# Kernel tuning notes

Measured on AMD Instinct MI355X. Metric: run time of the kernel, lower is better.

## Reference

```python
import jax, jax.numpy as jnp
import numpy as np

B, S, E, H, O = 256, 2048, 64, 128, 1


def setup_inputs() -> dict:
    key = jax.random.key(0)
    ks = jax.random.split(key, 12)
    s_e = 1.0 / np.sqrt(E)
    s_h = 1.0 / np.sqrt(H)
    return {
        "inputs": jax.random.normal(ks[0], (B, S, E), dtype=jnp.float32),
        "time_interval": jax.random.uniform(ks[1], (B, S), dtype=jnp.float32),
        "W_all": jax.random.uniform(ks[2], (4 * H, H), jnp.float32, -s_h, s_h),
        "b_all": jax.random.uniform(ks[3], (4 * H,), jnp.float32, -s_h, s_h),
        "U_all": jax.random.uniform(ks[4], (4 * H, E), jnp.float32, -s_e, s_e),
        "b_u": jax.random.uniform(ks[5], (4 * H,), jnp.float32, -s_e, s_e),
        "W_d": jax.random.uniform(ks[6], (H, H), jnp.float32, -s_h, s_h),
        "b_d": jax.random.uniform(ks[7], (H,), jnp.float32, -s_h, s_h),
        "W_out": jax.random.uniform(ks[8], (O, H), jnp.float32, -s_h, s_h),
        "b_out": jax.random.uniform(ks[9], (O,), jnp.float32, -s_h, s_h),
    }


def reference(inputs, time_interval, W_all, b_all, U_all, b_u, W_d, b_d, W_out, b_out):
    b, seq, _ = inputs.shape
    hdim = W_d.shape[0]
    # Precompute input projection for all timesteps: [S, B, 4H]
    x_proj = jnp.einsum('bse,fe->sbf', inputs, U_all) + b_u
    dt = time_interval.T  # [S, B]

    def step(carry, xs):
        h, c = carry
        xp, d = xs  # xp: [B,4H], d: [B]
        c_s1 = jnp.tanh(c @ W_d.T + b_d)
        c_adj = (c - c_s1) + c_s1 * d[:, None]
        outs = h @ W_all.T + b_all + xp
        f, i, o, c_tmp = jnp.split(outs, 4, axis=1)
        f = jax.nn.sigmoid(f)
        i = jax.nn.sigmoid(i)
        o = jax.nn.sigmoid(o)
        c_tmp = jax.nn.sigmoid(c_tmp)
        c_new = f * c_adj + i * c_tmp
        h_new = o * jnp.tanh(c_new)
        return (h_new, c_new), h_new

    h0 = jnp.zeros((b, hdim), dtype=inputs.dtype)
    c0 = jnp.zeros((b, hdim), dtype=inputs.dtype)
    _, hs = jax.lax.scan(step, (h0, c0), (x_proj, dt))  # hs: [S, B, H]
    # out(h_s) summed over s, then flatten to [B*O]
    outs = jnp.einsum('sbh,oh->sbo', hs, W_out) + b_out  # [S,B,O]
    return outs.sum(axis=0).reshape(-1)
```

## Files before the change

kernel.cpp:

```cpp
#include <hip/hip_runtime.h>
#include <math.h>

#define BB 256
#define SS 2048
#define EE 64
#define HH 128

typedef _Float16 half2_t __attribute__((ext_vector_type(2)));
typedef unsigned int uint2v __attribute__((ext_vector_type(2)));

#if defined(__has_builtin)
#if __has_builtin(__builtin_amdgcn_fdot2)
#define HAVE_FDOT2 1
#endif
#if __has_builtin(__builtin_amdgcn_update_dpp)
#define HAVE_DPP 1
#endif
#if __has_builtin(__builtin_amdgcn_permlane32_swap)
#define HAVE_PL32 1
#endif
#if __has_builtin(__builtin_amdgcn_exp2f)
#define EXP2F(x) __builtin_amdgcn_exp2f(x)
#else
#define EXP2F(x) exp2f(x)
#endif
#if __has_builtin(__builtin_amdgcn_rcpf)
#define RCPF(x) __builtin_amdgcn_rcpf(x)
#else
#define RCPF(x) (1.0f / (x))
#endif
#else
#define EXP2F(x) exp2f(x)
#define RCPF(x) (1.0f / (x))
#endif

__device__ __forceinline__ float dot2f(half2_t a, half2_t b, float c) {
#ifdef HAVE_FDOT2
    return __builtin_amdgcn_fdot2(a, b, c, false);
#else
    return c + (float)a.x * (float)b.x + (float)a.y * (float)b.y;
#endif
}

__device__ __forceinline__ float dpp_xor1(float v) {
#ifdef HAVE_DPP
    int r = __builtin_amdgcn_update_dpp(0, __float_as_int(v), 0xB1, 0xF, 0xF, true);
    return __int_as_float(r);
#else
    return __shfl_xor(v, 1, 64);
#endif
}
__device__ __forceinline__ float dpp_xor2(float v) {
#ifdef HAVE_DPP
    int r = __builtin_amdgcn_update_dpp(0, __float_as_int(v), 0x4E, 0xF, 0xF, true);
    return __int_as_float(r);
#else
    return __shfl_xor(v, 2, 64);
#endif
}

__device__ __forceinline__ float xhalf_recv(float a, float b, bool lower) {
#ifdef HAVE_PL32
    uint2v r = __builtin_amdgcn_permlane32_swap(__float_as_int(a), __float_as_int(b), false, false);
    return __int_as_float((int)(lower ? r.y : r.x));
#else
    float ra = __shfl_xor(a, 32, 64);
    float rb = __shfl_xor(b, 32, 64);
    return lower ? ra : rb;
#endif
}

__device__ __forceinline__ float sigm_f(float x) {
    float e = EXP2F(-1.442695041f * x);
    return RCPF(1.0f + e);
}
__device__ __forceinline__ float tanh_f(float x) {
    float e = EXP2F(2.885390082f * x);
    return 1.0f - 2.0f * RCPF(1.0f + e);
}

__global__ __attribute__((amdgpu_flat_work_group_size(512, 512)))
__attribute__((amdgpu_waves_per_eu(2, 2)))
void tlstm_fused8_kernel(
    const float* __restrict__ inputs,
    const float* __restrict__ time_interval,
    const float* __restrict__ W_all,
    const float* __restrict__ b_all,
    const float* __restrict__ U_all,
    const float* __restrict__ b_u,
    const float* __restrict__ W_d,
    const float* __restrict__ b_d,
    const float* __restrict__ W_out,
    const float* __restrict__ b_out,
    float* __restrict__ out)
{
    const int b  = blockIdx.x;
    const int t  = threadIdx.x;
    const int wv = t >> 6;
    const int lh = (t >> 5) & 1;
    const int k  = (t >> 2) & 7;
    const int m  = t & 3;
    const int L  = m + 4 * lh;
    const bool lower = (lh == 0);

    const int un_base = 16 * wv + 2 * k;
    const int my_un   = un_base + lh;

    __shared__ __align__(16) _Float16 sh_h[2][HH];
    __shared__ __align__(16) _Float16 sh_c[2][HH];
    __shared__ __align__(16) _Float16 sh_x[2][EE];
    __shared__ float sh_red[HH];

    half2_t wg[8][8];
    half2_t ug[8][4];
    half2_t wd[2][8];
    float   biasr, bd_r, wout_r;
    {
        #pragma unroll
        for (int uu = 0; uu < 2; ++uu) {
            #pragma unroll
            for (int q = 0; q < 4; ++q) {
                const int j   = q + 4 * uu;
                const int row = (un_base + uu) + 128 * q;
                const float4* pw = (const float4*)(W_all + (size_t)row * HH + 16 * L);
                #pragma unroll
                for (int i = 0; i < 4; ++i) {
                    float4 v = pw[i];
                    half2_t h0, h1;
                    h0.x = (_Float16)v.x; h0.y = (_Float16)v.y;
                    h1.x = (_Float16)v.z; h1.y = (_Float16)v.w;
                    wg[j][2*i]   = h0;
                    wg[j][2*i+1] = h1;
                }
                const float4* pu = (const float4*)(U_all + (size_t)row * EE + 8 * L);
                #pragma unroll
                for (int i = 0; i < 2; ++i) {
                    float4 v = pu[i];
                    half2_t h0, h1;
                    h0.x = (_Float16)v.x; h0.y = (_Float16)v.y;
                    h1.x = (_Float16)v.z; h1.y = (_Float16)v.w;
                    ug[j][2*i]   = h0;
                    ug[j][2*i+1] = h1;
                }
            }
            const int rowd = un_base + uu;
            const float4* pd = (const float4*)(W_d + (size_t)rowd * HH + 16 * L);
            #pragma unroll
            for (int i = 0; i < 4; ++i) {
                float4 v = pd[i];
                half2_t h0, h1;
                h0.x = (_Float16)v.x; h0.y = (_Float16)v.y;
                h1.x = (_Float16)v.z; h1.y = (_Float16)v.w;
                wd[uu][2*i]   = h0;
                wd[uu][2*i+1] = h1;
            }
        }
        const int row_own = my_un + 128 * m;
        biasr  = b_all[row_own] + b_u[row_own];
        bd_r   = b_d[my_un];
        wout_r = W_out[my_un];
    }

    const float* xg   = inputs + (size_t)b * SS * EE;
    const float* drow = time_interval + (size_t)b * SS;

    const int  xl   = t & 63;
    const bool xact = (xl < 8);
    const int  xidx = 8 * wv + (xl & 7);

    const _Float16* hb0 = &sh_h[0][16 * L];
    const _Float16* hb1 = &sh_h[1][16 * L];
    const _Float16* cb0 = &sh_c[0][16 * L];
    const _Float16* cb1 = &sh_c[1][16 * L];
    const _Float16* xr0 = &sh_x[0][8 * L];
    const _Float16* xr1 = &sh_x[1][8 * L];
    _Float16* wxp0 = &sh_x[0][xidx];
    _Float16* wxp1 = &sh_x[1][xidx];
    _Float16* wcp0 = &sh_c[0][my_un];
    _Float16* wcp1 = &sh_c[1][my_un];
    _Float16* whp0 = &sh_h[0][my_un];
    _Float16* whp1 = &sh_h[1][my_un];

    if (t < HH) { sh_h[0][t] = (_Float16)0.f; sh_c[0][t] = (_Float16)0.f; }
    float xcv = 0.f, xld = 0.f;
    if (xact) {
        sh_x[0][xidx] = (_Float16)xg[xidx];
        xcv = xg[EE + xidx];
        xld = xg[2 * EE + xidx];
    }
    float dv0 = drow[0], dv1 = drow[1], dv2 = drow[2];
    float hsum   = 0.f;
    float c_keep = 0.f;
    __syncthreads();

#define TLSTM_STEP(s, CUR, NXT)                                               \
    {                                                                         \
        if (xact) {                                                           \
            *wxp##NXT = (_Float16)xcv;                                        \
            xcv = xld;                                                        \
            const int s3 = ((s) + 3 < SS) ? (s) + 3 : SS - 1;                 \
            xld = xg[(size_t)s3 * EE + xidx];                                 \
        }                                                                     \
        float4 hv0, hv1, cv0, cv1, xv0;                                       \
        {                                                                     \
            const float4* hp = (const float4*)hb##CUR;                        \
            hv0 = hp[0]; hv1 = hp[1];                                         \
            const float4* cp = (const float4*)cb##CUR;                        \
            cv0 = cp[0]; cv1 = cp[1];                                         \
            const float4* xp = (const float4*)xr##CUR;                        \
            xv0 = xp[0];                                                      \
        }                                                                     \
        float a[8] = {0.f,0.f,0.f,0.f,0.f,0.f,0.f,0.f};                       \
        float ad0 = 0.f, ad1 = 0.f;                                           \
        {                                                                     \
            const half2_t* hh = (const half2_t*)&hv0;                         \
            _Pragma("unroll")                                                 \
            for (int p = 0; p < 4; ++p) {                                     \
                _Pragma("unroll")                                             \
                for (int j = 0; j < 8; ++j)                                   \
                    a[j] = dot2f(wg[j][p], hh[p], a[j]);                      \
            }                                                                 \
            hh = (const half2_t*)&hv1;                                        \
            _Pragma("unroll")                                                 \
            for (int p = 0; p < 4; ++p) {                                     \
                _Pragma("unroll")                                             \
                for (int j = 0; j < 8; ++j)                                   \
                    a[j] = dot2f(wg[j][4 + p], hh[p], a[j]);                  \
            }                                                                 \
            const half2_t* xh = (const half2_t*)&xv0;                         \
            _Pragma("unroll")                                                 \
            for (int p = 0; p < 4; ++p) {                                     \
                _Pragma("unroll")                                             \
                for (int j = 0; j < 8; ++j)                                   \
                    a[j] = dot2f(ug[j][p], xh[p], a[j]);                      \
            }                                                                 \
            const half2_t* ch = (const half2_t*)&cv0;                         \
            _Pragma("unroll")                                                 \
            for (int p = 0; p < 4; ++p) {                                     \
                ad0 = dot2f(wd[0][p], ch[p], ad0);                            \
                ad1 = dot2f(wd[1][p], ch[p], ad1);                            \
            }                                                                 \
            ch = (const half2_t*)&cv1;                                        \
            _Pragma("unroll")                                                 \
            for (int p = 0; p < 4; ++p) {                                     \
                ad0 = dot2f(wd[0][4 + p], ch[p], ad0);                        \
                ad1 = dot2f(wd[1][4 + p], ch[p], ad1);                        \
            }                                                                 \
        }                                                                     \
        \
        const bool oddl = (m & 1) != 0;                                       \
        const bool bit2 = (m & 2) != 0;                                       \
        float s0, s1, s2, s3v;                                                \
        {                                                                     \
            float snd, r;                                                     \
            snd = oddl ? a[0] : a[1]; r = dpp_xor1(snd);                      \
            s0 = (oddl ? a[1] : a[0]) + r;                                    \
            snd = oddl ? a[2] : a[3]; r = dpp_xor1(snd);                      \
            s1 = (oddl ? a[3] : a[2]) + r;                                    \
            snd = oddl ? a[4] : a[5]; r = dpp_xor1(snd);                      \
            s2 = (oddl ? a[5] : a[4]) + r;                                    \
            snd = oddl ? a[6] : a[7]; r = dpp_xor1(snd);                      \
            s3v = (oddl ? a[7] : a[6]) + r;                                   \
        }                                                                     \
        float u0v, u1v;                                                       \
        {                                                                     \
            float snd, r;                                                     \
            snd = bit2 ? s0 : s1; r = dpp_xor2(snd);                          \
            u0v = (bit2 ? s1 : s0) + r;                                       \
            snd = bit2 ? s2 : s3v; r = dpp_xor2(snd);                         \
            u1v = (bit2 ? s3v : s2) + r;                                      \
        }                                                                     \
        float g = (lower ? u0v : u1v) + xhalf_recv(u0v, u1v, lower);          \
        \
        float dd = (lower ? ad0 : ad1) + xhalf_recv(ad0, ad1, lower);         \
        dd += dpp_xor2(dd);                                                   \
        dd += dpp_xor1(dd);                                                   \
                  \
        float sg  = sigm_f(g + biasr);                                        \
        float cs1 = tanh_f(bd_r + dd);                                        \
        float sel1 = (m == 2) ? cs1 : sg;                                     \
        float sh2  = dpp_xor2(sel1);                \
        float sh2b = dpp_xor2(sg);                  \
        float dm1  = dv0 - 1.0f;                                              \
        float cadj = __builtin_fmaf(sh2, dm1, c_keep);   \
        float prod = sg * (oddl ? sh2 : cadj);      \
        float cn   = prod + dpp_xor1(prod);            \
        float hn   = sh2b * tanh_f(cn);                \
        c_keep = cn;                                                          \
        hsum  += hn;                                                          \
        if (m == 0) {                                                         \
            *wcp##NXT = (_Float16)cn;                                         \
            *whp##NXT = (_Float16)hn;                                         \
        }                                                                     \
        dv0 = dv1; dv1 = dv2;                                                 \
        const int sd = ((s) + 3 < SS) ? (s) + 3 : SS - 1;                     \
        dv2 = drow[sd];                                                       \
        __syncthreads();                                                      \
    }

    for (int s = 0; s < SS; s += 2) {
        TLSTM_STEP(s,     0, 1)
        TLSTM_STEP(s + 1, 1, 0)
    }
#undef TLSTM_STEP

    if (m == 0) sh_red[my_un] = hsum * wout_r;
    __syncthreads();
    if (t == 0) {
        float acc = 0.f;
        for (int i = 0; i < HH; ++i) acc += sh_red[i];
        out[b] = acc + (float)SS * b_out[0];
    }
}

extern "C" void kernel_launch(void* const* d_in, const int* in_sizes, int n_in,
                              void* d_out, int out_size, void* d_ws, size_t ws_size,
                              hipStream_t stream) {
    const float* inputs        = (const float*)d_in[0];
    const float* time_interval = (const float*)d_in[1];
    const float* W_all         = (const float*)d_in[2];
    const float* b_all         = (const float*)d_in[3];
    const float* U_all         = (const float*)d_in[4];
    const float* b_u           = (const float*)d_in[5];
    const float* W_d           = (const float*)d_in[6];
    const float* b_d           = (const float*)d_in[7];
    const float* W_out         = (const float*)d_in[8];
    const float* b_out         = (const float*)d_in[9];
    float* out = (float*)d_out;

    tlstm_fused8_kernel<<<dim3(BB), dim3(512), 0, stream>>>(
        inputs, time_interval, W_all, b_all, U_all, b_u,
        W_d, b_d, W_out, b_out, out);
}
```

Before: 1.787 ms.

## Split each hidden-unit dot product across 16 lanes with 1024-thread blocks

```diff
diff --git a/kernel.cpp b/kernel.cpp
--- a/kernel.cpp
+++ b/kernel.cpp
@@ -58,6 +58,14 @@
     return __shfl_xor(v, 2, 64);
 #endif
 }
+__device__ __forceinline__ float dpp_ror8(float v) {
+#ifdef HAVE_DPP
+    int r = __builtin_amdgcn_update_dpp(0, __float_as_int(v), 0x128, 0xF, 0xF, true);
+    return __int_as_float(r);
+#else
+    return __shfl_xor(v, 8, 64);
+#endif
+}
 
 __device__ __forceinline__ float xhalf_recv(float a, float b, bool lower) {
 #ifdef HAVE_PL32
@@ -79,9 +87,7 @@
     return 1.0f - 2.0f * RCPF(1.0f + e);
 }
 
-__global__ __attribute__((amdgpu_flat_work_group_size(512, 512)))
-__attribute__((amdgpu_waves_per_eu(2, 2)))
-void tlstm_fused8_kernel(
+__global__ __launch_bounds__(1024, 4) void tlstm_fused16_kernel(
     const float* __restrict__ inputs,
     const float* __restrict__ time_interval,
     const float* __restrict__ W_all,
@@ -96,14 +102,16 @@
 {
     const int b  = blockIdx.x;
     const int t  = threadIdx.x;
+    const int l  = t & 63;
     const int wv = t >> 6;
-    const int lh = (t >> 5) & 1;
-    const int k  = (t >> 2) & 7;
-    const int m  = t & 3;
-    const int L  = m + 4 * lh;
+    const int m  = l & 3;
+    const int q8 = (l >> 3) & 1;
+    const int lh = (l >> 5) & 1;
+    const int gidx = ((l >> 2) & 1) + 2 * ((l >> 4) & 1);
+    const int L  = m + 4 * q8 + 8 * lh;
     const bool lower = (lh == 0);
 
-    const int un_base = 16 * wv + 2 * k;
+    const int un_base = 8 * wv + 2 * gidx;
     const int my_un   = un_base + lh;
 
     __shared__ __align__(16) _Float16 sh_h[2][HH];
@@ -111,9 +119,9 @@
     __shared__ __align__(16) _Float16 sh_x[2][EE];
     __shared__ float sh_red[HH];
 
-    half2_t wg[8][8];
-    half2_t ug[8][4];
-    half2_t wd[2][8];
+    half2_t wg[8][4];
+    half2_t ug[8][2];
+    half2_t wd[2][4];
     float   biasr, bd_r, wout_r;
     {
         #pragma unroll
@@ -122,9 +130,9 @@
             for (int q = 0; q < 4; ++q) {
                 const int j   = q + 4 * uu;
                 const int row = (un_base + uu) + 128 * q;
-                const float4* pw = (const float4*)(W_all + (size_t)row * HH + 16 * L);
+                const float4* pw = (const float4*)(W_all + (size_t)row * HH + 8 * L);
                 #pragma unroll
-                for (int i = 0; i < 4; ++i) {
+                for (int i = 0; i < 2; ++i) {
                     float4 v = pw[i];
                     half2_t h0, h1;
                     h0.x = (_Float16)v.x; h0.y = (_Float16)v.y;
@@ -132,21 +140,20 @@
                     wg[j][2*i]   = h0;
                     wg[j][2*i+1] = h1;
                 }
-                const float4* pu = (const float4*)(U_all + (size_t)row * EE + 8 * L);
-                #pragma unroll
-                for (int i = 0; i < 2; ++i) {
-                    float4 v = pu[i];
+                const float4* pu = (const float4*)(U_all + (size_t)row * EE + 4 * L);
+                {
+                    float4 v = pu[0];
                     half2_t h0, h1;
                     h0.x = (_Float16)v.x; h0.y = (_Float16)v.y;
                     h1.x = (_Float16)v.z; h1.y = (_Float16)v.w;
-                    ug[j][2*i]   = h0;
-                    ug[j][2*i+1] = h1;
+                    ug[j][0] = h0;
+                    ug[j][1] = h1;
                 }
             }
             const int rowd = un_base + uu;
-            const float4* pd = (const float4*)(W_d + (size_t)rowd * HH + 16 * L);
+            const float4* pd = (const float4*)(W_d + (size_t)rowd * HH + 8 * L);
             #pragma unroll
-            for (int i = 0; i < 4; ++i) {
+            for (int i = 0; i < 2; ++i) {
                 float4 v = pd[i];
                 half2_t h0, h1;
                 h0.x = (_Float16)v.x; h0.y = (_Float16)v.y;
@@ -164,16 +171,15 @@
     const float* xg   = inputs + (size_t)b * SS * EE;
     const float* drow = time_interval + (size_t)b * SS;
 
-    const int  xl   = t & 63;
-    const bool xact = (xl < 8);
-    const int  xidx = 8 * wv + (xl & 7);
-
-    const _Float16* hb0 = &sh_h[0][16 * L];
-    const _Float16* hb1 = &sh_h[1][16 * L];
-    const _Float16* cb0 = &sh_c[0][16 * L];
-    const _Float16* cb1 = &sh_c[1][16 * L];
-    const _Float16* xr0 = &sh_x[0][8 * L];
-    const _Float16* xr1 = &sh_x[1][8 * L];
+    const bool xact = (l < 4);
+    const int  xidx = 4 * wv + (l & 3);
+
+    const _Float16* hb0 = &sh_h[0][8 * L];
+    const _Float16* hb1 = &sh_h[1][8 * L];
+    const _Float16* cb0 = &sh_c[0][8 * L];
+    const _Float16* cb1 = &sh_c[1][8 * L];
+    const _Float16* xr0 = &sh_x[0][4 * L];
+    const _Float16* xr1 = &sh_x[1][4 * L];
     _Float16* wxp0 = &sh_x[0][xidx];
     _Float16* wxp1 = &sh_x[1][xidx];
     _Float16* wcp0 = &sh_c[0][my_un];
@@ -201,53 +207,39 @@
             const int s3 = ((s) + 3 < SS) ? (s) + 3 : SS - 1;                 \
             xld = xg[(size_t)s3 * EE + xidx];                                 \
         }                                                                     \
-        float4 hv0, hv1, cv0, cv1, xv0;                                       \
+        float4 hv4, cv4f;                                                     \
+        float2 xv2;                                                           \
         {                                                                     \
-            const float4* hp = (const float4*)hb##CUR;                        \
-            hv0 = hp[0]; hv1 = hp[1];                                         \
-            const float4* cp = (const float4*)cb##CUR;                        \
-            cv0 = cp[0]; cv1 = cp[1];                                         \
-            const float4* xp = (const float4*)xr##CUR;                        \
-            xv0 = xp[0];                                                      \
+            hv4  = *(const float4*)hb##CUR;                                   \
+            cv4f = *(const float4*)cb##CUR;                                   \
+            xv2  = *(const float2*)xr##CUR;                                   \
         }                                                                     \
         float a[8] = {0.f,0.f,0.f,0.f,0.f,0.f,0.f,0.f};                       \
         float ad0 = 0.f, ad1 = 0.f;                                           \
         {                                                                     \
-            const half2_t* hh = (const half2_t*)&hv0;                         \
+            const half2_t* hh = (const half2_t*)&hv4;                         \
             _Pragma("unroll")                                                 \
             for (int p = 0; p < 4; ++p) {                                     \
                 _Pragma("unroll")                                             \
                 for (int j = 0; j < 8; ++j)                                   \
                     a[j] = dot2f(wg[j][p], hh[p], a[j]);                      \
             }                                                                 \
-            hh = (const half2_t*)&hv1;                                        \
+            const half2_t* xh = (const half2_t*)&xv2;                         \
             _Pragma("unroll")                                                 \
-            for (int p = 0; p < 4; ++p) {                                     \
-                _Pragma("unroll")                                             \
-                for (int j = 0; j < 8; ++j)                                   \
-                    a[j] = dot2f(wg[j][4 + p], hh[p], a[j]);                  \
-            }                                                                 \
-            const half2_t* xh = (const half2_t*)&xv0;                         \
-            _Pragma("unroll")                                                 \
-            for (int p = 0; p < 4; ++p) {                                     \
+            for (int p = 0; p < 2; ++p) {                                     \
                 _Pragma("unroll")                                             \
                 for (int j = 0; j < 8; ++j)                                   \
                     a[j] = dot2f(ug[j][p], xh[p], a[j]);                      \
             }                                                                 \
-            const half2_t* ch = (const half2_t*)&cv0;                         \
+            const half2_t* ch = (const half2_t*)&cv4f;                        \
             _Pragma("unroll")                                                 \
             for (int p = 0; p < 4; ++p) {                                     \
                 ad0 = dot2f(wd[0][p], ch[p], ad0);                            \
                 ad1 = dot2f(wd[1][p], ch[p], ad1);                            \
             }                                                                 \
-            ch = (const half2_t*)&cv1;                                        \
-            _Pragma("unroll")                                                 \
-            for (int p = 0; p < 4; ++p) {                                     \
-                ad0 = dot2f(wd[0][4 + p], ch[p], ad0);                        \
-                ad1 = dot2f(wd[1][4 + p], ch[p], ad1);                        \
-            }                                                                 \
-        }                                                                     \
-        \
+        }                                                                     \
+          \
+                   \
         const bool oddl = (m & 1) != 0;                                       \
         const bool bit2 = (m & 2) != 0;                                       \
         float s0, s1, s2, s3v;                                                \
@@ -270,9 +262,12 @@
             snd = bit2 ? s2 : s3v; r = dpp_xor2(snd);                         \
             u1v = (bit2 ? s3v : s2) + r;                                      \
         }                                                                     \
+        u0v += dpp_ror8(u0v);                                                 \
+        u1v += dpp_ror8(u1v);                                                 \
         float g = (lower ? u0v : u1v) + xhalf_recv(u0v, u1v, lower);          \
-        \
+                        \
         float dd = (lower ? ad0 : ad1) + xhalf_recv(ad0, ad1, lower);         \
+        dd += dpp_ror8(dd);                                                   \
         dd += dpp_xor2(dd);                                                   \
         dd += dpp_xor1(dd);                                                   \
                   \
@@ -288,7 +283,7 @@
         float hn   = sh2b * tanh_f(cn);                \
         c_keep = cn;                                                          \
         hsum  += hn;                                                          \
-        if (m == 0) {                                                         \
+        if ((l & 11) == 0) {          \
             *wcp##NXT = (_Float16)cn;                                         \
             *whp##NXT = (_Float16)hn;                                         \
         }                                                                     \
@@ -304,7 +299,7 @@
     }
 #undef TLSTM_STEP
 
-    if (m == 0) sh_red[my_un] = hsum * wout_r;
+    if ((l & 11) == 0) sh_red[my_un] = hsum * wout_r;
     __syncthreads();
     if (t == 0) {
         float acc = 0.f;
@@ -328,7 +323,7 @@
     const float* b_out         = (const float*)d_in[9];
     float* out = (float*)d_out;
 
-    tlstm_fused8_kernel<<<dim3(BB), dim3(512), 0, stream>>>(
+    tlstm_fused16_kernel<<<dim3(BB), dim3(1024), 0, stream>>>(
         inputs, time_interval, W_all, b_all, U_all, b_u,
         W_d, b_d, W_out, b_out, out);
 }
```

New measurement: 2.307 ms. +29.1%, slower.
